# Optimization experiments

Hardware: AMD Instinct MI355X
Metric: run time of the kernel (lower is better)

Reference implementation:

```python
import jax, jax.numpy as jnp
import numpy as np

T = 200000


def _sine_layer(tvec, A, w, phi, phic, wc):
    # tvec: (t,), A/w/phi: (n,1), phic/wc: (1,)
    phi_static = jax.nn.relu(phic)  # (1,)
    w_static = jax.nn.relu(wc)
    ph = jax.nn.relu(phi) + phi_static  # (n,1)
    ww = jax.nn.relu(w) + w_static
    sine = A * jnp.sin(ww * tvec[None, :] + ph)  # (n,t)
    return sine, phi_static, w_static


def _selector_layer(tvec, wave_input, w, phi, phic, wc, phi_prev, w_prev):
    # wave_input: (n,t), w/phi: (m,n), phic/wc/phi_prev/w_prev: (1,)
    # NOTE: phi_prev/w_prev passed but phi_prev flag is False in the network,
    # so they are NOT added (matches torch: `if self.phi_prev and ...`).
    phi_static = jax.nn.relu(phic)
    w_static = jax.nn.relu(wc)
    ph = (jax.nn.relu(phi) + phi_static)[:, :, None]  # (m,n,1)
    ww = (jax.nn.relu(w) + w_static)[:, :, None]
    sine = 0.5 * jnp.sin(ww * tvec[None, None, :] + ph) + 0.5  # (m,n,t)
    out = jnp.einsum('mnt,nt->mt', sine, wave_input)  # (m,t)
    return out, phi_static, w_static


def setup_inputs() -> dict:
    key = jax.random.key(0)
    ks = jax.random.split(key, 18)
    r = lambda k, s: jax.random.normal(k, s, dtype=jnp.float32)
    return {
        'initial_wave_input': r(ks[0], (20, T)),
        'A0': r(ks[1], (20, 1)), 'w0': r(ks[2], (20, 1)), 'phi0': r(ks[3], (20, 1)),
        'wc0': r(ks[4], (1,)), 'phic0': r(ks[5], (1,)),
        'w1': r(ks[6], (25, 20)), 'phi1': r(ks[7], (25, 20)),
        'wc1': r(ks[8], (1,)), 'phic1': r(ks[9], (1,)),
        'w2': r(ks[10], (30, 25)), 'phi2': r(ks[11], (30, 25)),
        'wc2': r(ks[12], (1,)), 'phic2': r(ks[13], (1,)),
        'w3': r(ks[14], (1, 30)), 'phi3': r(ks[15], (1, 30)),
        'wc3': r(ks[16], (1,)), 'phic3': r(ks[17], (1,)),
    }


def reference(initial_wave_input, A0, w0, phi0, wc0, phic0,
              w1, phi1, wc1, phic1, w2, phi2, wc2, phic2,
              w3, phi3, wc3, phic3):
    tvec = jnp.linspace(1.0, 1000.0, T, dtype=jnp.float32)
    # initial_wave_input is an argument of the torch module but is never used.
    s, phi, w = _sine_layer(tvec, A0, w0, phi0, phic0, wc0)
    s, phi, w = _selector_layer(tvec, s, w1, phi1, phic1, wc1, phi, w)
    s, phi, w = _selector_layer(tvec, s, w2, phi2, phic2, wc2, phi, w)
    s, phi, w = _selector_layer(tvec, s, w3, phi3, phic3, wc3, phi, w)
    return s  # (1, t)
```

## Files before the change

kernel.cpp:

```cpp
#include <hip/hip_runtime.h>
#include <hip/hip_bf16.h>

#define T_TOTAL 200000
#define INV2PI 0.15915494309189535f

__device__ float g_P[2840];

__device__ __forceinline__ float relu_f(float x) { return fmaxf(x, 0.0f); }

__device__ __forceinline__ float sin_rev(float rev) {
    return __builtin_amdgcn_sinf(__builtin_amdgcn_fractf(rev));
}

__global__ void prep_kernel(
    const float* __restrict__ A0,
    const float* __restrict__ w0, const float* __restrict__ phi0,
    const float* __restrict__ wc0, const float* __restrict__ phic0,
    const float* __restrict__ w1, const float* __restrict__ phi1,
    const float* __restrict__ wc1, const float* __restrict__ phic1,
    const float* __restrict__ w2, const float* __restrict__ phi2,
    const float* __restrict__ wc2, const float* __restrict__ phic2,
    const float* __restrict__ w3, const float* __restrict__ phi3,
    const float* __restrict__ wc3, const float* __restrict__ phic3)
{
    const int tid = blockIdx.x * blockDim.x + threadIdx.x;
    const int stride = blockDim.x * gridDim.x;

    const float ws0 = relu_f(wc0[0]), ps0 = relu_f(phic0[0]);
    const float ws1 = relu_f(wc1[0]), ps1 = relu_f(phic1[0]);
    const float ws2 = relu_f(wc2[0]), ps2 = relu_f(phic2[0]);
    const float ws3 = relu_f(wc3[0]), ps3 = relu_f(phic3[0]);

    for (int n = tid; n < 20; n += stride) {
        g_P[2 * n]     = (relu_f(w0[n])   + ws0) * INV2PI;
        g_P[2 * n + 1] = (relu_f(phi0[n]) + ps0) * INV2PI;
        g_P[40 + n]    = A0[n];
    }
    for (int k = tid; k < 20 * 28; k += stride) {
        const int n = k / 28, m = k % 28;
        const int d = 60 + 2 * k;
        if (m < 25) {
            const int s = m * 20 + n;
            g_P[d]     = (relu_f(w1[s])   + ws1) * INV2PI;
            g_P[d + 1] = (relu_f(phi1[s]) + ps1) * INV2PI;
        } else {
            g_P[d] = 0.0f; g_P[d + 1] = 0.0f;
        }
    }
    for (int k = tid; k < 25 * 32; k += stride) {
        const int n = k / 32, m = k % 32;
        const int d = 1180 + 2 * k;
        if (m < 30) {
            const int s = m * 25 + n;
            g_P[d]     = (relu_f(w2[s])   + ws2) * INV2PI;
            g_P[d + 1] = (relu_f(phi2[s]) + ps2) * INV2PI;
        } else {
            g_P[d] = 0.0f; g_P[d + 1] = 0.0f;
        }
    }
    for (int k = tid; k < 30; k += stride) {
        g_P[2780 + 2 * k]     = (relu_f(w3[k])   + ws3) * INV2PI;
        g_P[2780 + 2 * k + 1] = (relu_f(phi3[k]) + ps3) * INV2PI;
    }
}

__launch_bounds__(256)
__global__ void wave_main(float* __restrict__ out)
{
    __shared__ float sh0[20 * 64];
    __shared__ float sh1[25 * 64];
    __shared__ float sh2[30 * 64];

    const int tid = threadIdx.x;
    const int l = tid & 63;
    const int w = __builtin_amdgcn_readfirstlane(tid >> 6);
    const int t = blockIdx.x * 64 + l;
    const float tv = fmaf((float)t, 999.0f / 199999.0f, 1.0f);

    {
        const float* __restrict__ p = &g_P[10 * w];
        const float* __restrict__ a = &g_P[40 + 5 * w];
#pragma unroll
        for (int i = 0; i < 5; ++i) {
            float rev = fmaf(p[2 * i], tv, p[2 * i + 1]);
            sh0[(5 * w + i) * 64 + l] = a[i] * sin_rev(rev);
        }
    }
    __syncthreads();

    float acc1[7];
#pragma unroll
    for (int j = 0; j < 7; ++j) acc1[j] = 0.0f;
    float sum0 = 0.0f;
#pragma clang loop unroll(disable)
    for (int n = 0; n < 20; ++n) {
        const float s0n = sh0[n * 64 + l];
        sum0 += s0n;
        const float* __restrict__ p = &g_P[60 + 56 * n + 14 * w];
#pragma unroll
        for (int j = 0; j < 7; ++j) {
            float rev = fmaf(p[2 * j], tv, p[2 * j + 1]);
            acc1[j] = fmaf(sin_rev(rev), s0n, acc1[j]);
        }
    }
#pragma unroll
    for (int j = 0; j < 7; ++j) {
        const int m = 7 * w + j;
        if (m < 25) sh1[m * 64 + l] = fmaf(0.5f, acc1[j], 0.5f * sum0);
    }
    __syncthreads();

    float acc2[8];
#pragma unroll
    for (int j = 0; j < 8; ++j) acc2[j] = 0.0f;
    float sum1 = 0.0f;
#pragma clang loop unroll(disable)
    for (int n = 0; n < 25; ++n) {
        const float s1n = sh1[n * 64 + l];
        sum1 += s1n;
        const float* __restrict__ p = &g_P[1180 + 64 * n + 16 * w];
#pragma unroll
        for (int j = 0; j < 8; ++j) {
            float rev = fmaf(p[2 * j], tv, p[2 * j + 1]);
            acc2[j] = fmaf(sin_rev(rev), s1n, acc2[j]);
        }
    }
#pragma unroll
    for (int j = 0; j < 8; ++j) {
        const int m = 8 * w + j;
        if (m < 30) sh2[m * 64 + l] = fmaf(0.5f, acc2[j], 0.5f * sum1);
    }
    __syncthreads();

    if (w == 0) {
        float acc3 = 0.0f, sum2 = 0.0f;
#pragma unroll
        for (int n = 0; n < 30; ++n) {
            const float s2n = sh2[n * 64 + l];
            sum2 += s2n;
            float rev = fmaf(g_P[2780 + 2 * n], tv, g_P[2780 + 2 * n + 1]);
            acc3 = fmaf(sin_rev(rev), s2n, acc3);
        }
        out[t] = fmaf(0.5f, acc3, 0.5f * sum2);
    }
}

extern "C" void kernel_launch(void* const* d_in, const int* in_sizes, int n_in,
                              void* d_out, int out_size, void* d_ws, size_t ws_size,
                              hipStream_t stream) {
    (void)in_sizes; (void)n_in; (void)d_ws; (void)ws_size; (void)out_size;
    const float* A0    = (const float*)d_in[1];
    const float* w0    = (const float*)d_in[2];
    const float* phi0  = (const float*)d_in[3];
    const float* wc0   = (const float*)d_in[4];
    const float* phic0 = (const float*)d_in[5];
    const float* w1    = (const float*)d_in[6];
    const float* phi1  = (const float*)d_in[7];
    const float* wc1   = (const float*)d_in[8];
    const float* phic1 = (const float*)d_in[9];
    const float* w2    = (const float*)d_in[10];
    const float* phi2  = (const float*)d_in[11];
    const float* wc2   = (const float*)d_in[12];
    const float* phic2 = (const float*)d_in[13];
    const float* w3    = (const float*)d_in[14];
    const float* phi3  = (const float*)d_in[15];
    const float* wc3   = (const float*)d_in[16];
    const float* phic3 = (const float*)d_in[17];

    float* out = (float*)d_out;

    hipLaunchKernelGGL(prep_kernel, dim3(11), dim3(256), 0, stream,
                       A0, w0, phi0, wc0, phic0,
                       w1, phi1, wc1, phic1,
                       w2, phi2, wc2, phic2,
                       w3, phi3, wc3, phic3);

    const int grid = T_TOTAL / 64;
    hipLaunchKernelGGL(wave_main, dim3(grid), dim3(256), 0, stream, out);
}
```

Before: 53.51 us.

## Replace hardware sine with packed-FP32 polynomial cosine in selector layers

The selector layers now compute sin(2πx) as cos(2π(x−0.25)) with a degree-6 even polynomial in (frac−0.5)², evaluated with 2-wide float vectors so the compiler can emit packed FP32 FMA/mul instructions. The parameter table is relaid out so frequency and phase are stored in separate contiguous 32-wide halves, allowing vector loads, and the phase absorbs the +0.25 shift. This avoids the quarter-rate transcendental sine unit in the hot loops, at the cost of more ALU ops per sine and a possible small accuracy difference. Layer 1 work per wave grows from 7 to 8 outputs, with padded lanes.

Result: slower. 71.66 us (+33.9%).

```diff
diff --git a/kernel.cpp b/kernel.cpp
--- a/kernel.cpp
+++ b/kernel.cpp
@@ -4,12 +4,36 @@
 #define T_TOTAL 200000
 #define INV2PI 0.15915494309189535f
 
-__device__ float g_P[2840];
+typedef float v2f __attribute__((ext_vector_type(2)));
+
+__device__ float g_P[3000];
 
 __device__ __forceinline__ float relu_f(float x) { return fmaxf(x, 0.0f); }
 
 __device__ __forceinline__ float sin_rev(float rev) {
     return __builtin_amdgcn_sinf(__builtin_amdgcn_fractf(rev));
+}
+
+__device__ __forceinline__ v2f sin2pi_pk(v2f rev) {
+    v2f g;
+    g[0] = __builtin_amdgcn_fractf(rev[0]);
+    g[1] = __builtin_amdgcn_fractf(rev[1]);
+    v2f h = g - 0.5f;
+    v2f u = h * h;
+    const float B6 =  7.9035364f;
+    const float B5 = -26.4262568f;
+    const float B4 =  60.2446414f;
+    const float B3 = -85.4568172f;
+    const float B2 =  64.9393940f;
+    const float B1 = -19.7392088f;
+    const float B0 =  1.0f;
+    v2f p = u * B6 + B5;
+    p = p * u + B4;
+    p = p * u + B3;
+    p = p * u + B2;
+    p = p * u + B1;
+    p = p * u + B0;
+    return p;
 }
 
 __global__ void prep_kernel(
@@ -36,31 +60,31 @@
         g_P[2 * n + 1] = (relu_f(phi0[n]) + ps0) * INV2PI;
         g_P[40 + n]    = A0[n];
     }
-    for (int k = tid; k < 20 * 28; k += stride) {
-        const int n = k / 28, m = k % 28;
-        const int d = 60 + 2 * k;
+    for (int k = tid; k < 20 * 32; k += stride) {
+        const int n = k >> 5, m = k & 31;
+        float wwv = 0.0f, phv = 0.25f;
         if (m < 25) {
             const int s = m * 20 + n;
-            g_P[d]     = (relu_f(w1[s])   + ws1) * INV2PI;
-            g_P[d + 1] = (relu_f(phi1[s]) + ps1) * INV2PI;
-        } else {
-            g_P[d] = 0.0f; g_P[d + 1] = 0.0f;
-        }
+            wwv = (relu_f(w1[s])   + ws1) * INV2PI;
+            phv = (relu_f(phi1[s]) + ps1) * INV2PI + 0.25f;
+        }
+        g_P[60 + 64 * n + m]      = wwv;
+        g_P[60 + 64 * n + 32 + m] = phv;
     }
     for (int k = tid; k < 25 * 32; k += stride) {
-        const int n = k / 32, m = k % 32;
-        const int d = 1180 + 2 * k;
+        const int n = k >> 5, m = k & 31;
+        float wwv = 0.0f, phv = 0.25f;
         if (m < 30) {
             const int s = m * 25 + n;
-            g_P[d]     = (relu_f(w2[s])   + ws2) * INV2PI;
-            g_P[d + 1] = (relu_f(phi2[s]) + ps2) * INV2PI;
-        } else {
-            g_P[d] = 0.0f; g_P[d + 1] = 0.0f;
-        }
+            wwv = (relu_f(w2[s])   + ws2) * INV2PI;
+            phv = (relu_f(phi2[s]) + ps2) * INV2PI + 0.25f;
+        }
+        g_P[1340 + 64 * n + m]      = wwv;
+        g_P[1340 + 64 * n + 32 + m] = phv;
     }
     for (int k = tid; k < 30; k += stride) {
-        g_P[2780 + 2 * k]     = (relu_f(w3[k])   + ws3) * INV2PI;
-        g_P[2780 + 2 * k + 1] = (relu_f(phi3[k]) + ps3) * INV2PI;
+        g_P[2940 + 2 * k]     = (relu_f(w3[k])   + ws3) * INV2PI;
+        g_P[2940 + 2 * k + 1] = (relu_f(phi3[k]) + ps3) * INV2PI;
     }
 }
 
@@ -76,6 +100,7 @@
     const int w = __builtin_amdgcn_readfirstlane(tid >> 6);
     const int t = blockIdx.x * 64 + l;
     const float tv = fmaf((float)t, 999.0f / 199999.0f, 1.0f);
+    v2f tv2; tv2[0] = tv; tv2[1] = tv;
 
     {
         const float* __restrict__ p = &g_P[10 * w];
@@ -88,47 +113,55 @@
     }
     __syncthreads();
 
-    float acc1[7];
-#pragma unroll
-    for (int j = 0; j < 7; ++j) acc1[j] = 0.0f;
+    v2f acc1[4] = {};
     float sum0 = 0.0f;
 #pragma clang loop unroll(disable)
     for (int n = 0; n < 20; ++n) {
         const float s0n = sh0[n * 64 + l];
         sum0 += s0n;
-        const float* __restrict__ p = &g_P[60 + 56 * n + 14 * w];
-#pragma unroll
-        for (int j = 0; j < 7; ++j) {
-            float rev = fmaf(p[2 * j], tv, p[2 * j + 1]);
-            acc1[j] = fmaf(sin_rev(rev), s0n, acc1[j]);
-        }
-    }
-#pragma unroll
-    for (int j = 0; j < 7; ++j) {
-        const int m = 7 * w + j;
-        if (m < 25) sh1[m * 64 + l] = fmaf(0.5f, acc1[j], 0.5f * sum0);
+        v2f s0d; s0d[0] = s0n; s0d[1] = s0n;
+        const v2f* __restrict__ wwp = (const v2f*)&g_P[60 + 64 * n + 8 * w];
+        const v2f* __restrict__ php = (const v2f*)&g_P[60 + 64 * n + 32 + 8 * w];
+#pragma unroll
+        for (int j = 0; j < 4; ++j) {
+            v2f rev = wwp[j] * tv2 + php[j];
+            v2f sn = sin2pi_pk(rev);
+            acc1[j] = sn * s0d + acc1[j];
+        }
+    }
+#pragma unroll
+    for (int j = 0; j < 4; ++j) {
+#pragma unroll
+        for (int c = 0; c < 2; ++c) {
+            const int m = 8 * w + 2 * j + c;
+            if (m < 25) sh1[m * 64 + l] = fmaf(0.5f, acc1[j][c], 0.5f * sum0);
+        }
     }
     __syncthreads();
 
-    float acc2[8];
-#pragma unroll
-    for (int j = 0; j < 8; ++j) acc2[j] = 0.0f;
+    v2f acc2[4] = {};
     float sum1 = 0.0f;
 #pragma clang loop unroll(disable)
     for (int n = 0; n < 25; ++n) {
         const float s1n = sh1[n * 64 + l];
         sum1 += s1n;
-        const float* __restrict__ p = &g_P[1180 + 64 * n + 16 * w];
-#pragma unroll
-        for (int j = 0; j < 8; ++j) {
-            float rev = fmaf(p[2 * j], tv, p[2 * j + 1]);
-            acc2[j] = fmaf(sin_rev(rev), s1n, acc2[j]);
-        }
-    }
-#pragma unroll
-    for (int j = 0; j < 8; ++j) {
-        const int m = 8 * w + j;
-        if (m < 30) sh2[m * 64 + l] = fmaf(0.5f, acc2[j], 0.5f * sum1);
+        v2f s1d; s1d[0] = s1n; s1d[1] = s1n;
+        const v2f* __restrict__ wwp = (const v2f*)&g_P[1340 + 64 * n + 8 * w];
+        const v2f* __restrict__ php = (const v2f*)&g_P[1340 + 64 * n + 32 + 8 * w];
+#pragma unroll
+        for (int j = 0; j < 4; ++j) {
+            v2f rev = wwp[j] * tv2 + php[j];
+            v2f sn = sin2pi_pk(rev);
+            acc2[j] = sn * s1d + acc2[j];
+        }
+    }
+#pragma unroll
+    for (int j = 0; j < 4; ++j) {
+#pragma unroll
+        for (int c = 0; c < 2; ++c) {
+            const int m = 8 * w + 2 * j + c;
+            if (m < 30) sh2[m * 64 + l] = fmaf(0.5f, acc2[j][c], 0.5f * sum1);
+        }
     }
     __syncthreads();
 
@@ -138,7 +171,7 @@
         for (int n = 0; n < 30; ++n) {
             const float s2n = sh2[n * 64 + l];
             sum2 += s2n;
-            float rev = fmaf(g_P[2780 + 2 * n], tv, g_P[2780 + 2 * n + 1]);
+            float rev = fmaf(g_P[2940 + 2 * n], tv, g_P[2940 + 2 * n + 1]);
             acc3 = fmaf(sin_rev(rev), s2n, acc3);
         }
         out[t] = fmaf(0.5f, acc3, 0.5f * sum2);
```
